# Optimization experiments

Measured on AMD Instinct MI355X. Metric: run time of the kernel, lower is better.

The kernel has to match this reference:

```python
import jax, jax.numpy as jnp
import numpy as np

N_QUBITS = 10
QLCU_LAYERS = 2
FEATURE_DIM = 256
BATCH = 256
N_PARAMS = 5 * N_QUBITS * QLCU_LAYERS  # 100
TWO_PI = 2.0 * np.pi


def _rx_mat(theta):
    # (B,) -> (B,2,2) complex64
    c = jnp.cos(theta / 2).astype(jnp.complex64)
    s = (-1j * jnp.sin(theta / 2)).astype(jnp.complex64)
    return jnp.stack([jnp.stack([c, s], -1), jnp.stack([s, c], -1)], -2)


def _ry_mat(theta):
    c = jnp.cos(theta / 2).astype(jnp.complex64)
    s = jnp.sin(theta / 2).astype(jnp.complex64)
    return jnp.stack([jnp.stack([c, -s], -1), jnp.stack([s, c], -1)], -2)


def _rz_mat(theta):
    e0 = jnp.exp(-0.5j * theta.astype(jnp.complex64))
    e1 = jnp.exp(0.5j * theta.astype(jnp.complex64))
    z = jnp.zeros_like(e0)
    return jnp.stack([jnp.stack([e0, z], -1), jnp.stack([z, e1], -1)], -2)


def _apply_1q(state, U, w):
    # state: (B,)+(2,)*n ; U: (B,2,2) ; wire w (PennyLane wire 0 = most significant)
    s = jnp.moveaxis(state, 1 + w, -1)
    s = jnp.einsum('bij,b...j->b...i', U, s)
    return jnp.moveaxis(s, -1, 1 + w)


def _apply_crx(state, theta, c, t):
    # controlled-RX: apply RX(theta) on target t where control c == 1
    s = jnp.moveaxis(state, (1 + c, 1 + t), (-2, -1))
    U = _rx_mat(theta)
    s1 = jnp.einsum('bij,b...j->b...i', U, s[..., 1, :])
    s = jnp.stack([s[..., 0, :], s1], axis=-2)
    return jnp.moveaxis(s, (-2, -1), (1 + c, 1 + t))


def _circuit(params):
    # params: (B, N_PARAMS) angles. Returns (B, 3*n) expvals [X.., Y.., Z..]
    n = N_QUBITS
    B = params.shape[0]
    state = jnp.zeros((B,) + (2,) * n, jnp.complex64)
    state = state.at[(slice(None),) + (0,) * n].set(1.0)
    idx = 0
    for _ in range(QLCU_LAYERS):
        for i in range(n):
            state = _apply_1q(state, _rx_mat(params[:, idx]), i)
            state = _apply_1q(state, _ry_mat(params[:, idx + 1]), i)
            state = _apply_1q(state, _rz_mat(params[:, idx + 2]), i)
            idx += 3
        for i in range(n):
            state = _apply_crx(state, params[:, idx], i, (i + 1) % n)
            idx += 1
        for i in range(n - 1, -1, -1):
            state = _apply_crx(state, params[:, idx], i, (i - 1) % n)
            idx += 1
    X, Y, Z = [], [], []
    for w in range(n):
        s = jnp.moveaxis(state, 1 + w, -1).reshape(B, -1, 2)
        z01 = jnp.sum(jnp.conj(s[..., 0]) * s[..., 1], axis=1)  # (B,)
        X.append(2.0 * jnp.real(z01))
        Y.append(2.0 * jnp.imag(z01))
        probs = jnp.sum(jnp.abs(s) ** 2, axis=1)  # (B,2)
        Z.append(probs[:, 0] - probs[:, 1])
    return jnp.stack(X + Y + Z, axis=1).astype(jnp.float32)


def _branch(x, W, b, base):
    p = x @ W.T + b            # (B, N_PARAMS)
    p = p + base[None, :]
    p = jax.nn.sigmoid(p) * TWO_PI
    return _circuit(p)


def setup_inputs() -> dict:
    key = jax.random.key(0)
    ks = jax.random.split(key, 16)
    d = {
        'x': jax.random.normal(ks[0], (BATCH, FEATURE_DIM), jnp.float32),
        'W1': jax.random.normal(ks[1], (N_PARAMS, FEATURE_DIM), jnp.float32) * 0.05,
        'b1': jnp.zeros((N_PARAMS,), jnp.float32),
        'W2': jax.random.normal(ks[2], (N_PARAMS, FEATURE_DIM), jnp.float32) * 0.05,
        'b2': jnp.zeros((N_PARAMS,), jnp.float32),
        'W3': jax.random.normal(ks[3], (N_PARAMS, FEATURE_DIM), jnp.float32) * 0.05,
        'b3': jnp.zeros((N_PARAMS,), jnp.float32),
        'base1': jax.random.uniform(ks[4], (N_PARAMS,), jnp.float32) * TWO_PI,
        'base2': jax.random.uniform(ks[5], (N_PARAMS,), jnp.float32) * TWO_PI,
        'base3': jax.random.uniform(ks[6], (N_PARAMS,), jnp.float32) * TWO_PI,
        'alpha_real': jax.random.uniform(ks[7], (1,), jnp.float32),
        'alpha_imag': jnp.zeros((1,), jnp.float32),
        'beta_real': jax.random.uniform(ks[8], (1,), jnp.float32),
        'beta_imag': jnp.zeros((1,), jnp.float32),
        'gamma_real': jax.random.uniform(ks[9], (1,), jnp.float32),
        'gamma_imag': jnp.zeros((1,), jnp.float32),
    }
    return d


def reference(x, W1, b1, W2, b2, W3, b3, base1, base2, base3,
              alpha_real, alpha_imag, beta_real, beta_imag, gamma_real, gamma_imag):
    m1 = _branch(x, W1, b1, base1)  # (B, 3n)
    m2 = _branch(x, W2, b2, base2)
    m3 = _branch(x, W3, b3, base3)
    norm = jnp.sqrt(alpha_real**2 + alpha_imag**2 + beta_real**2 + beta_imag**2
                    + gamma_real**2 + gamma_imag**2 + 1e-9)
    ar, ai = alpha_real / norm, alpha_imag / norm
    br, bi = beta_real / norm, beta_imag / norm
    gr, gi = gamma_real / norm, gamma_imag / norm
    re = ar * m1 + br * m2 + gr * m3
    im = ai * m1 + bi * m2 + gi * m3
    return jnp.sqrt(re * re + im * im)
```

## Files before the change

kernel.cpp:

```cpp
#include <hip/hip_runtime.h>
#include <math.h>

#define NQ 10
#define NPAR 100
#define FDIM 256
#define BATCH 256
#define NOUT 30
#define TWO_PI_F 6.283185307179586f


__device__ __forceinline__ float shx(float v, int mask) {
    return __shfl_xor(v, mask, 64);
}

__device__ __forceinline__ float2 cmul(float2 a, float2 b) {
    return make_float2(a.x*b.x - a.y*b.y, a.x*b.y + a.y*b.x);
}

template<int BIT>
__device__ __forceinline__ void gate1q(float2 (&st)[16], int lane,
                                       float2 u00, float2 u01, float2 u10, float2 u11)
{
    if constexpr (BIT >= 6) {
        constexpr int rb = 1 << (BIT - 6);
        #pragma unroll
        for (int a = 0; a < 16; ++a) {
            if (a & rb) continue;
            const int a1 = a | rb;
            const float2 A0 = st[a], A1 = st[a1];
            float2 n0, n1;
            n0.x = u00.x*A0.x - u00.y*A0.y + u01.x*A1.x - u01.y*A1.y;
            n0.y = u00.x*A0.y + u00.y*A0.x + u01.x*A1.y + u01.y*A1.x;
            n1.x = u10.x*A0.x - u10.y*A0.y + u11.x*A1.x - u11.y*A1.y;
            n1.y = u10.x*A0.y + u10.y*A0.x + u11.x*A1.y + u11.y*A1.x;
            st[a] = n0; st[a1] = n1;
        }
    } else {
        constexpr int lb = 1 << BIT;
        const bool hi = (lane & lb) != 0;
        const float2 A = hi ? u11 : u00;
        const float2 B = hi ? u10 : u01;
        #pragma unroll
        for (int a = 0; a < 16; ++a) {
            const float2 m = st[a];
            float2 p;
            p.x = shx(m.x, lb); p.y = shx(m.y, lb);
            float2 n;
            n.x = A.x*m.x - A.y*m.y + B.x*p.x - B.y*p.y;
            n.y = A.x*m.y + A.y*m.x + B.x*p.y + B.y*p.x;
            st[a] = n;
        }
    }
}

template<int BC, int BT>
__device__ __forceinline__ void crx(float2 (&st)[16], int lane, float c, float s)
{
    if constexpr (BT >= 6) {
        constexpr int rt = 1 << (BT - 6);
        if constexpr (BC >= 6) {
            constexpr int rc = 1 << (BC - 6);
            #pragma unroll
            for (int a = 0; a < 16; ++a) {
                if (!(a & rc) || (a & rt)) continue;
                const int a1 = a | rt;
                const float2 A0 = st[a], A1 = st[a1];
                float2 n0, n1;
                n0.x = c*A0.x + s*A1.y;  n0.y = c*A0.y - s*A1.x;
                n1.x = c*A1.x + s*A0.y;  n1.y = c*A1.y - s*A0.x;
                st[a] = n0; st[a1] = n1;
            }
        } else {
            constexpr int lc = 1 << BC;
            const bool act = (lane & lc) != 0;
            const float cc = act ? c : 1.f;
            const float ss = act ? s : 0.f;
            #pragma unroll
            for (int a = 0; a < 16; ++a) {
                if (a & rt) continue;
                const int a1 = a | rt;
                const float2 A0 = st[a], A1 = st[a1];
                float2 n0, n1;
                n0.x = cc*A0.x + ss*A1.y;  n0.y = cc*A0.y - ss*A1.x;
                n1.x = cc*A1.x + ss*A0.y;  n1.y = cc*A1.y - ss*A0.x;
                st[a] = n0; st[a1] = n1;
            }
        }
    } else {
        constexpr int lt = 1 << BT;
        float cc, ss;
        if constexpr (BC < 6) {
            constexpr int lc = 1 << BC;
            const bool act = (lane & lc) != 0;
            cc = act ? c : 1.f;
            ss = act ? s : 0.f;
        } else { cc = c; ss = s; }
        #pragma unroll
        for (int a = 0; a < 16; ++a) {
            if constexpr (BC >= 6) {
                constexpr int rc = 1 << (BC - 6);
                if (!(a & rc)) continue;
            }
            const float2 m = st[a];
            float2 p;
            p.x = shx(m.x, lt); p.y = shx(m.y, lt);
            float2 n;
            n.x = cc*m.x + ss*p.y;
            n.y = cc*m.y - ss*p.x;
            st[a] = n;
        }
    }
}

template<int Q>
__device__ __forceinline__ void layer1q(float2 (&st)[16], int lane, const float2* cs, int idx)
{
    if constexpr (Q < NQ) {
        const float2 X = cs[idx], Y = cs[idx + 1], Z = cs[idx + 2];
        const float cx = X.x, sx = X.y, cy = Y.x, sy = Y.y, cz = Z.x, sz = Z.y;
        const float2 m00 = make_float2( cy*cx,  sy*sx);
        const float2 m01 = make_float2(-sy*cx, -cy*sx);
        const float2 m10 = make_float2( sy*cx, -cy*sx);
        const float2 m11 = make_float2( cy*cx, -sy*sx);
        const float2 u00 = make_float2(cz*m00.x + sz*m00.y, cz*m00.y - sz*m00.x);
        const float2 u01 = make_float2(cz*m01.x + sz*m01.y, cz*m01.y - sz*m01.x);
        const float2 u10 = make_float2(cz*m10.x - sz*m10.y, cz*m10.y + sz*m10.x);
        const float2 u11 = make_float2(cz*m11.x - sz*m11.y, cz*m11.y + sz*m11.x);
        gate1q<9 - Q>(st, lane, u00, u01, u10, u11);
        layer1q<Q + 1>(st, lane, cs, idx + 3);
    }
}

template<int Q>
__device__ __forceinline__ void ringF(float2 (&st)[16], int lane, const float2* cs, int idx)
{
    if constexpr (Q < NQ) {
        const float2 p = cs[idx];
        crx<9 - Q, 9 - ((Q + 1) % NQ)>(st, lane, p.x, p.y);
        ringF<Q + 1>(st, lane, cs, idx + 1);
    }
}

template<int Q>
__device__ __forceinline__ void ringB(float2 (&st)[16], int lane, const float2* cs, int idx)
{
    if constexpr (Q >= 0) {
        const float2 p = cs[idx];
        crx<9 - Q, 9 - ((Q + NQ - 1) % NQ)>(st, lane, p.x, p.y);
        ringB<Q - 1>(st, lane, cs, idx + 1);
    }
}

__device__ __forceinline__ void col0(const float2* cs, int w, float2& u00, float2& u10)
{
    const float2 X = cs[3*w], Y = cs[3*w + 1], Z = cs[3*w + 2];
    const float cx = X.x, sx = X.y, cy = Y.x, sy = Y.y, cz = Z.x, sz = Z.y;
    const float2 m00 = make_float2(cy*cx,  sy*sx);
    const float2 m10 = make_float2(sy*cx, -cy*sx);
    u00 = make_float2(cz*m00.x + sz*m00.y, cz*m00.y - sz*m00.x);
    u10 = make_float2(cz*m10.x - sz*m10.y, cz*m10.y + sz*m10.x);
}

template<int W>
__device__ __forceinline__ void measureAll(const float2 (&st)[16], int lane, float* m_row)
{
    if constexpr (W < NQ) {
        constexpr int B = 9 - W;
        float sre = 0.f, smm = 0.f, szz = 0.f;
        if constexpr (B >= 6) {
            constexpr int rb = 1 << (B - 6);
            #pragma unroll
            for (int a = 0; a < 16; ++a) {
                if (a & rb) continue;
                const int a1 = a | rb;
                const float2 A0 = st[a], A1 = st[a1];
                sre += A0.x*A1.x + A0.y*A1.y;
                smm += A0.x*A1.y - A0.y*A1.x;
                szz += A0.x*A0.x + A0.y*A0.y - A1.x*A1.x - A1.y*A1.y;
            }
            sre *= 2.f; smm *= 2.f;
        } else {
            constexpr int lb = 1 << B;
            const float sgn = (lane & lb) ? -1.f : 1.f;
            #pragma unroll
            for (int a = 0; a < 16; ++a) {
                const float2 m = st[a];
                float2 p;
                p.x = shx(m.x, lb); p.y = shx(m.y, lb);
                sre += m.x*p.x + m.y*p.y;
                smm += sgn * (m.x*p.y - m.y*p.x);
                szz += sgn * (m.x*m.x + m.y*m.y - p.x*p.x - p.y*p.y);
            }
            szz *= 0.5f;
        }
        #pragma unroll
        for (int off = 1; off < 64; off <<= 1) {
            sre += shx(sre, off);
            smm += shx(smm, off);
            szz += shx(szz, off);
        }
        if (lane == 0) {
            m_row[W]      = sre;
            m_row[10 + W] = smm;
            m_row[20 + W] = szz;
        }
        measureAll<W + 1>(st, lane, m_row);
    }
}

__global__ __launch_bounds__(192) void qsb_fused(
    const float* __restrict__ x,
    const float* __restrict__ W1, const float* __restrict__ b1, const float* __restrict__ base1,
    const float* __restrict__ W2, const float* __restrict__ b2, const float* __restrict__ base2,
    const float* __restrict__ W3, const float* __restrict__ b3, const float* __restrict__ base3,
    const float* __restrict__ ar_, const float* __restrict__ ai_,
    const float* __restrict__ br_, const float* __restrict__ bi_,
    const float* __restrict__ gr_, const float* __restrict__ gi_,
    float* __restrict__ out)
{
    const int b    = blockIdx.x;
    const int wv   = threadIdx.x >> 6;
    const int lane = threadIdx.x & 63;

    const float* W    = (wv == 0) ? W1    : (wv == 1) ? W2    : W3;
    const float* bias = (wv == 0) ? b1    : (wv == 1) ? b2    : b3;
    const float* base = (wv == 0) ? base1 : (wv == 1) ? base2 : base3;

    __shared__ float2 css[3][NPAR];
    __shared__ float  mloc[3][NOUT];
    float2* cs = css[wv];

    if (lane < 50) {
        const int p0 = 2 * lane;
        const float4* xr = reinterpret_cast<const float4*>(x + (size_t)b * FDIM);
        const float4* w0 = reinterpret_cast<const float4*>(W + (size_t)p0 * FDIM);
        const float4* w1 = reinterpret_cast<const float4*>(W + (size_t)(p0 + 1) * FDIM);
        float acc0 = 0.f, acc1 = 0.f;
        #pragma unroll 8
        for (int k = 0; k < FDIM / 4; ++k) {
            const float4 xv = xr[k];
            const float4 a  = w0[k];
            const float4 bb = w1[k];
            acc0 += xv.x*a.x  + xv.y*a.y  + xv.z*a.z  + xv.w*a.w;
            acc1 += xv.x*bb.x + xv.y*bb.y + xv.z*bb.z + xv.w*bb.w;
        }
        acc0 += bias[p0]     + base[p0];
        acc1 += bias[p0 + 1] + base[p0 + 1];
        const float t0 = TWO_PI_F / (1.f + __expf(-acc0));
        const float t1 = TWO_PI_F / (1.f + __expf(-acc1));
        float s0, c0, s1, c1;
        __sincosf(0.5f * t0, &s0, &c0);
        __sincosf(0.5f * t1, &s1, &c1);
        cs[p0]     = make_float2(c0, s0);
        cs[p0 + 1] = make_float2(c1, s1);
    }
    __syncthreads();

    float2 st[16];
    {
        float2 lp = make_float2(1.f, 0.f);
        #pragma unroll
        for (int bb = 0; bb < 6; ++bb) {
            float2 u00, u10;
            col0(cs, 9 - bb, u00, u10);
            const float2 sel = ((lane >> bb) & 1) ? u10 : u00;
            lp = cmul(lp, sel);
        }
        float2 v3[2], v2[2], v1[2], v0[2];
        col0(cs, 3, v3[0], v3[1]);
        col0(cs, 2, v2[0], v2[1]);
        col0(cs, 1, v1[0], v1[1]);
        col0(cs, 0, v0[0], v0[1]);
        #pragma unroll
        for (int a = 0; a < 16; ++a) {
            float2 t = cmul(v3[a & 1], v2[(a >> 1) & 1]);
            t = cmul(t, cmul(v1[(a >> 2) & 1], v0[(a >> 3) & 1]));
            st[a] = cmul(t, lp);
        }
    }

    ringF<0>(st, lane, cs, 30);
    ringB<NQ - 1>(st, lane, cs, 40);
    layer1q<0>(st, lane, cs, 50);
    ringF<0>(st, lane, cs, 80);
    ringB<NQ - 1>(st, lane, cs, 90);

    measureAll<0>(st, lane, mloc[wv]);
    __syncthreads();

    if (threadIdx.x < NOUT) {
        const int i = threadIdx.x;
        const float ar = ar_[0], ai = ai_[0];
        const float br = br_[0], bi = bi_[0];
        const float gr = gr_[0], gi = gi_[0];
        const float inv = 1.f / sqrtf(ar*ar + ai*ai + br*br + bi*bi
                                      + gr*gr + gi*gi + 1e-9f);
        const float m1 = mloc[0][i], m2 = mloc[1][i], m3 = mloc[2][i];
        const float re = (ar * m1 + br * m2 + gr * m3) * inv;
        const float im = (ai * m1 + bi * m2 + gi * m3) * inv;
        out[(size_t)b * NOUT + i] = sqrtf(re * re + im * im);
    }
}

extern "C" void kernel_launch(void* const* d_in, const int* in_sizes, int n_in,
                              void* d_out, int out_size, void* d_ws, size_t ws_size,
                              hipStream_t stream)
{
    (void)in_sizes; (void)n_in; (void)out_size; (void)d_ws; (void)ws_size;
    const float* x     = (const float*)d_in[0];
    const float* W1    = (const float*)d_in[1];
    const float* b1    = (const float*)d_in[2];
    const float* W2    = (const float*)d_in[3];
    const float* b2    = (const float*)d_in[4];
    const float* W3    = (const float*)d_in[5];
    const float* b3    = (const float*)d_in[6];
    const float* base1 = (const float*)d_in[7];
    const float* base2 = (const float*)d_in[8];
    const float* base3 = (const float*)d_in[9];
    const float* ar    = (const float*)d_in[10];
    const float* ai    = (const float*)d_in[11];
    const float* br    = (const float*)d_in[12];
    const float* bi    = (const float*)d_in[13];
    const float* gr    = (const float*)d_in[14];
    const float* gi    = (const float*)d_in[15];

    qsb_fused<<<dim3(BATCH), dim3(192), 0, stream>>>(
        x, W1, b1, base1, W2, b2, base2, W3, b3, base3,
        ar, ai, br, bi, gr, gi, (float*)d_out);
}
```

Baseline: 117.3 us.

## Split each circuit state across two wavefronts and use DPP/swizzle lane exchanges

Each branch's 1024-amplitude state is now split across two wavefronts with 8 slots per lane instead of one wavefront with 16. Qubit 9 becomes the wave index, and gates on it exchange amplitudes through shared memory with block barriers. Shuffle-xor is replaced by DPP and ds_swizzle intrinsics for lane masks below 32. The linear projection is spread over 100 threads and the measurement reduction now produces four partial sums per branch. The goal is more parallelism and lower register pressure, at the cost of many __syncthreads on the qubit-9 gates.

```diff
diff --git a/kernel.cpp b/kernel.cpp
--- a/kernel.cpp
+++ b/kernel.cpp
@@ -7,24 +7,161 @@
 #define BATCH 256
 #define NOUT 30
 #define TWO_PI_F 6.283185307179586f
-
-
-__device__ __forceinline__ float shx(float v, int mask) {
-    return __shfl_xor(v, mask, 64);
+#define NSLOT 8
+
+
+template<int MASK>
+__device__ __forceinline__ float lx(float v) {
+    if constexpr (MASK == 1) {
+        return __int_as_float(__builtin_amdgcn_update_dpp(
+            0, __float_as_int(v), 0xB1, 0xF, 0xF, true));
+    } else if constexpr (MASK == 2) {
+        return __int_as_float(__builtin_amdgcn_update_dpp(
+            0, __float_as_int(v), 0x4E, 0xF, 0xF, true));
+    } else if constexpr (MASK == 8) {
+        return __int_as_float(__builtin_amdgcn_update_dpp(
+            0, __float_as_int(v), 0x128, 0xF, 0xF, true));
+    } else if constexpr (MASK == 4) {
+        return __int_as_float(__builtin_amdgcn_ds_swizzle(__float_as_int(v), 0x101F));
+    } else if constexpr (MASK == 16) {
+        return __int_as_float(__builtin_amdgcn_ds_swizzle(__float_as_int(v), 0x401F));
+    } else {
+        return __shfl_xor(v, 32, 64);
+    }
+}
+
+template<int MASK>
+__device__ __forceinline__ float2 lx2(float2 v) {
+    return make_float2(lx<MASK>(v.x), lx<MASK>(v.y));
 }
 
 __device__ __forceinline__ float2 cmul(float2 a, float2 b) {
     return make_float2(a.x*b.x - a.y*b.y, a.x*b.y + a.y*b.x);
 }
 
+struct Ctx {
+    int lane;
+    int W;
+    float2* exs;
+    float2* exp_;
+};
+
+template<int BC, int BT>
+__device__ __forceinline__ void crx(float2 (&st)[NSLOT], const Ctx& cx, float c, float s)
+{
+    if constexpr (BT == 9) {
+        if constexpr (BC >= 6) {
+            constexpr int rc = 1 << (BC - 6);
+            #pragma unroll
+            for (int a = 0; a < NSLOT; ++a) if (a & rc) cx.exs[a] = st[a];
+            __syncthreads();
+            #pragma unroll
+            for (int a = 0; a < NSLOT; ++a) if (a & rc) {
+                const float2 p = cx.exp_[a]; const float2 m = st[a];
+                st[a] = make_float2(c*m.x + s*p.y, c*m.y - s*p.x);
+            }
+            __syncthreads();
+        } else {
+            #pragma unroll
+            for (int a = 0; a < NSLOT; ++a) cx.exs[a] = st[a];
+            __syncthreads();
+            const bool act = (cx.lane >> BC) & 1;
+            const float cc = act ? c : 1.f, ss = act ? s : 0.f;
+            #pragma unroll
+            for (int a = 0; a < NSLOT; ++a) {
+                const float2 p = cx.exp_[a]; const float2 m = st[a];
+                st[a] = make_float2(cc*m.x + ss*p.y, cc*m.y - ss*p.x);
+            }
+            __syncthreads();
+        }
+    } else if constexpr (BC == 9) {
+        if (cx.W) {
+            if constexpr (BT >= 6) {
+                constexpr int rt = 1 << (BT - 6);
+                #pragma unroll
+                for (int a = 0; a < NSLOT; ++a) {
+                    if (a & rt) continue;
+                    const int a1 = a | rt;
+                    const float2 A0 = st[a], A1 = st[a1];
+                    st[a]  = make_float2(c*A0.x + s*A1.y, c*A0.y - s*A1.x);
+                    st[a1] = make_float2(c*A1.x + s*A0.y, c*A1.y - s*A0.x);
+                }
+            } else {
+                constexpr int M = 1 << BT;
+                #pragma unroll
+                for (int a = 0; a < NSLOT; ++a) {
+                    const float2 p = lx2<M>(st[a]); const float2 m = st[a];
+                    st[a] = make_float2(c*m.x + s*p.y, c*m.y - s*p.x);
+                }
+            }
+        }
+    } else if constexpr (BT >= 6) {
+        constexpr int rt = 1 << (BT - 6);
+        if constexpr (BC >= 6) {
+            constexpr int rc = 1 << (BC - 6);
+            #pragma unroll
+            for (int a = 0; a < NSLOT; ++a) {
+                if (!(a & rc) || (a & rt)) continue;
+                const int a1 = a | rt;
+                const float2 A0 = st[a], A1 = st[a1];
+                st[a]  = make_float2(c*A0.x + s*A1.y, c*A0.y - s*A1.x);
+                st[a1] = make_float2(c*A1.x + s*A0.y, c*A1.y - s*A0.x);
+            }
+        } else {
+            const bool act = (cx.lane >> BC) & 1;
+            const float cc = act ? c : 1.f, ss = act ? s : 0.f;
+            #pragma unroll
+            for (int a = 0; a < NSLOT; ++a) {
+                if (a & rt) continue;
+                const int a1 = a | rt;
+                const float2 A0 = st[a], A1 = st[a1];
+                st[a]  = make_float2(cc*A0.x + ss*A1.y, cc*A0.y - ss*A1.x);
+                st[a1] = make_float2(cc*A1.x + ss*A0.y, cc*A1.y - ss*A0.x);
+            }
+        }
+    } else {
+        constexpr int M = 1 << BT;
+        if constexpr (BC >= 6) {
+            constexpr int rc = 1 << (BC - 6);
+            #pragma unroll
+            for (int a = 0; a < NSLOT; ++a) {
+                if (!(a & rc)) continue;
+                const float2 p = lx2<M>(st[a]); const float2 m = st[a];
+                st[a] = make_float2(c*m.x + s*p.y, c*m.y - s*p.x);
+            }
+        } else {
+            const bool act = (cx.lane >> BC) & 1;
+            const float cc = act ? c : 1.f, ss = act ? s : 0.f;
+            #pragma unroll
+            for (int a = 0; a < NSLOT; ++a) {
+                const float2 p = lx2<M>(st[a]); const float2 m = st[a];
+                st[a] = make_float2(cc*m.x + ss*p.y, cc*m.y - ss*p.x);
+            }
+        }
+    }
+}
+
 template<int BIT>
-__device__ __forceinline__ void gate1q(float2 (&st)[16], int lane,
+__device__ __forceinline__ void gate1q(float2 (&st)[NSLOT], const Ctx& cx,
                                        float2 u00, float2 u01, float2 u10, float2 u11)
 {
-    if constexpr (BIT >= 6) {
+    if constexpr (BIT == 9) {
+        #pragma unroll
+        for (int a = 0; a < NSLOT; ++a) cx.exs[a] = st[a];
+        __syncthreads();
+        const float2 A = cx.W ? u11 : u00;
+        const float2 B = cx.W ? u10 : u01;
+        #pragma unroll
+        for (int a = 0; a < NSLOT; ++a) {
+            const float2 m = st[a]; const float2 p = cx.exp_[a];
+            st[a] = make_float2(A.x*m.x - A.y*m.y + B.x*p.x - B.y*p.y,
+                                A.x*m.y + A.y*m.x + B.x*p.y + B.y*p.x);
+        }
+        __syncthreads();
+    } else if constexpr (BIT >= 6) {
         constexpr int rb = 1 << (BIT - 6);
         #pragma unroll
-        for (int a = 0; a < 16; ++a) {
+        for (int a = 0; a < NSLOT; ++a) {
             if (a & rb) continue;
             const int a1 = a | rb;
             const float2 A0 = st[a], A1 = st[a1];
@@ -36,118 +173,58 @@
             st[a] = n0; st[a1] = n1;
         }
     } else {
-        constexpr int lb = 1 << BIT;
-        const bool hi = (lane & lb) != 0;
+        constexpr int M = 1 << BIT;
+        const bool hi = (cx.lane >> BIT) & 1;
         const float2 A = hi ? u11 : u00;
         const float2 B = hi ? u10 : u01;
         #pragma unroll
-        for (int a = 0; a < 16; ++a) {
-            const float2 m = st[a];
-            float2 p;
-            p.x = shx(m.x, lb); p.y = shx(m.y, lb);
-            float2 n;
-            n.x = A.x*m.x - A.y*m.y + B.x*p.x - B.y*p.y;
-            n.y = A.x*m.y + A.y*m.x + B.x*p.y + B.y*p.x;
-            st[a] = n;
-        }
-    }
-}
-
-template<int BC, int BT>
-__device__ __forceinline__ void crx(float2 (&st)[16], int lane, float c, float s)
-{
-    if constexpr (BT >= 6) {
-        constexpr int rt = 1 << (BT - 6);
-        if constexpr (BC >= 6) {
-            constexpr int rc = 1 << (BC - 6);
-            #pragma unroll
-            for (int a = 0; a < 16; ++a) {
-                if (!(a & rc) || (a & rt)) continue;
-                const int a1 = a | rt;
-                const float2 A0 = st[a], A1 = st[a1];
-                float2 n0, n1;
-                n0.x = c*A0.x + s*A1.y;  n0.y = c*A0.y - s*A1.x;
-                n1.x = c*A1.x + s*A0.y;  n1.y = c*A1.y - s*A0.x;
-                st[a] = n0; st[a1] = n1;
-            }
-        } else {
-            constexpr int lc = 1 << BC;
-            const bool act = (lane & lc) != 0;
-            const float cc = act ? c : 1.f;
-            const float ss = act ? s : 0.f;
-            #pragma unroll
-            for (int a = 0; a < 16; ++a) {
-                if (a & rt) continue;
-                const int a1 = a | rt;
-                const float2 A0 = st[a], A1 = st[a1];
-                float2 n0, n1;
-                n0.x = cc*A0.x + ss*A1.y;  n0.y = cc*A0.y - ss*A1.x;
-                n1.x = cc*A1.x + ss*A0.y;  n1.y = cc*A1.y - ss*A0.x;
-                st[a] = n0; st[a1] = n1;
-            }
-        }
-    } else {
-        constexpr int lt = 1 << BT;
-        float cc, ss;
-        if constexpr (BC < 6) {
-            constexpr int lc = 1 << BC;
-            const bool act = (lane & lc) != 0;
-            cc = act ? c : 1.f;
-            ss = act ? s : 0.f;
-        } else { cc = c; ss = s; }
-        #pragma unroll
-        for (int a = 0; a < 16; ++a) {
-            if constexpr (BC >= 6) {
-                constexpr int rc = 1 << (BC - 6);
-                if (!(a & rc)) continue;
-            }
-            const float2 m = st[a];
-            float2 p;
-            p.x = shx(m.x, lt); p.y = shx(m.y, lt);
-            float2 n;
-            n.x = cc*m.x + ss*p.y;
-            n.y = cc*m.y - ss*p.x;
-            st[a] = n;
+        for (int a = 0; a < NSLOT; ++a) {
+            const float2 p = lx2<M>(st[a]); const float2 m = st[a];
+            st[a] = make_float2(A.x*m.x - A.y*m.y + B.x*p.x - B.y*p.y,
+                                A.x*m.y + A.y*m.x + B.x*p.y + B.y*p.x);
         }
     }
 }
 
 template<int Q>
-__device__ __forceinline__ void layer1q(float2 (&st)[16], int lane, const float2* cs, int idx)
+__device__ __forceinline__ void layer1q(float2 (&st)[NSLOT], const Ctx& cx,
+                                        const float2* cs, int idx)
 {
     if constexpr (Q < NQ) {
         const float2 X = cs[idx], Y = cs[idx + 1], Z = cs[idx + 2];
-        const float cx = X.x, sx = X.y, cy = Y.x, sy = Y.y, cz = Z.x, sz = Z.y;
-        const float2 m00 = make_float2( cy*cx,  sy*sx);
-        const float2 m01 = make_float2(-sy*cx, -cy*sx);
-        const float2 m10 = make_float2( sy*cx, -cy*sx);
-        const float2 m11 = make_float2( cy*cx, -sy*sx);
+        const float cx_ = X.x, sx = X.y, cy = Y.x, sy = Y.y, cz = Z.x, sz = Z.y;
+        const float2 m00 = make_float2( cy*cx_,  sy*sx);
+        const float2 m01 = make_float2(-sy*cx_, -cy*sx);
+        const float2 m10 = make_float2( sy*cx_, -cy*sx);
+        const float2 m11 = make_float2( cy*cx_, -sy*sx);
         const float2 u00 = make_float2(cz*m00.x + sz*m00.y, cz*m00.y - sz*m00.x);
         const float2 u01 = make_float2(cz*m01.x + sz*m01.y, cz*m01.y - sz*m01.x);
         const float2 u10 = make_float2(cz*m10.x - sz*m10.y, cz*m10.y + sz*m10.x);
         const float2 u11 = make_float2(cz*m11.x - sz*m11.y, cz*m11.y + sz*m11.x);
-        gate1q<9 - Q>(st, lane, u00, u01, u10, u11);
-        layer1q<Q + 1>(st, lane, cs, idx + 3);
+        gate1q<9 - Q>(st, cx, u00, u01, u10, u11);
+        layer1q<Q + 1>(st, cx, cs, idx + 3);
     }
 }
 
 template<int Q>
-__device__ __forceinline__ void ringF(float2 (&st)[16], int lane, const float2* cs, int idx)
+__device__ __forceinline__ void ringF(float2 (&st)[NSLOT], const Ctx& cx,
+                                      const float2* cs, int idx)
 {
     if constexpr (Q < NQ) {
         const float2 p = cs[idx];
-        crx<9 - Q, 9 - ((Q + 1) % NQ)>(st, lane, p.x, p.y);
-        ringF<Q + 1>(st, lane, cs, idx + 1);
+        crx<9 - Q, 9 - ((Q + 1) % NQ)>(st, cx, p.x, p.y);
+        ringF<Q + 1>(st, cx, cs, idx + 1);
     }
 }
 
 template<int Q>
-__device__ __forceinline__ void ringB(float2 (&st)[16], int lane, const float2* cs, int idx)
+__device__ __forceinline__ void ringB(float2 (&st)[NSLOT], const Ctx& cx,
+                                      const float2* cs, int idx)
 {
     if constexpr (Q >= 0) {
         const float2 p = cs[idx];
-        crx<9 - Q, 9 - ((Q + NQ - 1) % NQ)>(st, lane, p.x, p.y);
-        ringB<Q - 1>(st, lane, cs, idx + 1);
+        crx<9 - Q, 9 - ((Q + NQ - 1) % NQ)>(st, cx, p.x, p.y);
+        ringB<Q - 1>(st, cx, cs, idx + 1);
     }
 }
 
@@ -161,16 +238,30 @@
     u10 = make_float2(cz*m10.x - sz*m10.y, cz*m10.y + sz*m10.x);
 }
 
-template<int W>
-__device__ __forceinline__ void measureAll(const float2 (&st)[16], int lane, float* m_row)
-{
-    if constexpr (W < NQ) {
-        constexpr int B = 9 - W;
+template<int Wq>
+__device__ __forceinline__ void measureAll(const float2 (&st)[NSLOT], const Ctx& cx,
+                                           float* mrow )
+{
+    if constexpr (Wq < NQ) {
+        constexpr int B = 9 - Wq;
         float sre = 0.f, smm = 0.f, szz = 0.f;
-        if constexpr (B >= 6) {
+        if constexpr (B == 9) {
+            #pragma unroll
+            for (int a = 0; a < NSLOT; ++a) cx.exs[a] = st[a];
+            __syncthreads();
+            const float sgn = cx.W ? -1.f : 1.f;
+            #pragma unroll
+            for (int a = 0; a < NSLOT; ++a) {
+                const float2 m = st[a], p = cx.exp_[a];
+                sre += m.x*p.x + m.y*p.y;
+                smm += sgn * (m.x*p.y - m.y*p.x);
+                szz += sgn * (m.x*m.x + m.y*m.y);
+            }
+            __syncthreads();
+        } else if constexpr (B >= 6) {
             constexpr int rb = 1 << (B - 6);
             #pragma unroll
-            for (int a = 0; a < 16; ++a) {
+            for (int a = 0; a < NSLOT; ++a) {
                 if (a & rb) continue;
                 const int a1 = a | rb;
                 const float2 A0 = st[a], A1 = st[a1];
@@ -180,35 +271,32 @@
             }
             sre *= 2.f; smm *= 2.f;
         } else {
-            constexpr int lb = 1 << B;
-            const float sgn = (lane & lb) ? -1.f : 1.f;
-            #pragma unroll
-            for (int a = 0; a < 16; ++a) {
+            constexpr int M = 1 << B;
+            const float sgn = ((cx.lane >> B) & 1) ? -1.f : 1.f;
+            #pragma unroll
+            for (int a = 0; a < NSLOT; ++a) {
                 const float2 m = st[a];
-                float2 p;
-                p.x = shx(m.x, lb); p.y = shx(m.y, lb);
+                const float2 p = lx2<M>(m);
                 sre += m.x*p.x + m.y*p.y;
                 smm += sgn * (m.x*p.y - m.y*p.x);
                 szz += sgn * (m.x*m.x + m.y*m.y - p.x*p.x - p.y*p.y);
             }
             szz *= 0.5f;
         }
-        #pragma unroll
-        for (int off = 1; off < 64; off <<= 1) {
-            sre += shx(sre, off);
-            smm += shx(smm, off);
-            szz += shx(szz, off);
-        }
-        if (lane == 0) {
-            m_row[W]      = sre;
-            m_row[10 + W] = smm;
-            m_row[20 + W] = szz;
-        }
-        measureAll<W + 1>(st, lane, m_row);
-    }
-}
-
-__global__ __launch_bounds__(192) void qsb_fused(
+        sre += lx<1>(sre); sre += lx<2>(sre); sre += lx<4>(sre); sre += lx<8>(sre); sre += lx<16>(sre);
+        smm += lx<1>(smm); smm += lx<2>(smm); smm += lx<4>(smm); smm += lx<8>(smm); smm += lx<16>(smm);
+        szz += lx<1>(szz); szz += lx<2>(szz); szz += lx<4>(szz); szz += lx<8>(szz); szz += lx<16>(szz);
+        if ((cx.lane & 31) == 0) {
+            const int k = (cx.W << 1) | (cx.lane >> 5);
+            mrow[k * NOUT + Wq]      = sre;
+            mrow[k * NOUT + 10 + Wq] = smm;
+            mrow[k * NOUT + 20 + Wq] = szz;
+        }
+        measureAll<Wq + 1>(st, cx, mrow);
+    }
+}
+
+__global__ __launch_bounds__(384) void qsb_fused(
     const float* __restrict__ x,
     const float* __restrict__ W1, const float* __restrict__ b1, const float* __restrict__ base1,
     const float* __restrict__ W2, const float* __restrict__ b2, const float* __restrict__ base2,
@@ -219,86 +307,91 @@
     float* __restrict__ out)
 {
     const int b    = blockIdx.x;
-    const int wv   = threadIdx.x >> 6;
+    const int wv2  = threadIdx.x >> 6;
+    const int br   = wv2 >> 1;
+    const int W    = wv2 & 1;
     const int lane = threadIdx.x & 63;
-
-    const float* W    = (wv == 0) ? W1    : (wv == 1) ? W2    : W3;
-    const float* bias = (wv == 0) ? b1    : (wv == 1) ? b2    : b3;
-    const float* base = (wv == 0) ? base1 : (wv == 1) ? base2 : base3;
+    const int lt   = (W << 6) | lane;
+
+    const float* Wp   = (br == 0) ? W1    : (br == 1) ? W2    : W3;
+    const float* bias = (br == 0) ? b1    : (br == 1) ? b2    : b3;
+    const float* base = (br == 0) ? base1 : (br == 1) ? base2 : base3;
 
     __shared__ float2 css[3][NPAR];
-    __shared__ float  mloc[3][NOUT];
-    float2* cs = css[wv];
-
-    if (lane < 50) {
-        const int p0 = 2 * lane;
+    __shared__ float2 exb[3][2][64][9];
+    __shared__ float  mred[3][4][NOUT];
+
+    if (lt < NPAR) {
         const float4* xr = reinterpret_cast<const float4*>(x + (size_t)b * FDIM);
-        const float4* w0 = reinterpret_cast<const float4*>(W + (size_t)p0 * FDIM);
-        const float4* w1 = reinterpret_cast<const float4*>(W + (size_t)(p0 + 1) * FDIM);
-        float acc0 = 0.f, acc1 = 0.f;
+        const float4* wr = reinterpret_cast<const float4*>(Wp + (size_t)lt * FDIM);
+        float acc = 0.f;
         #pragma unroll 8
         for (int k = 0; k < FDIM / 4; ++k) {
             const float4 xv = xr[k];
-            const float4 a  = w0[k];
-            const float4 bb = w1[k];
-            acc0 += xv.x*a.x  + xv.y*a.y  + xv.z*a.z  + xv.w*a.w;
-            acc1 += xv.x*bb.x + xv.y*bb.y + xv.z*bb.z + xv.w*bb.w;
-        }
-        acc0 += bias[p0]     + base[p0];
-        acc1 += bias[p0 + 1] + base[p0 + 1];
-        const float t0 = TWO_PI_F / (1.f + __expf(-acc0));
-        const float t1 = TWO_PI_F / (1.f + __expf(-acc1));
-        float s0, c0, s1, c1;
-        __sincosf(0.5f * t0, &s0, &c0);
-        __sincosf(0.5f * t1, &s1, &c1);
-        cs[p0]     = make_float2(c0, s0);
-        cs[p0 + 1] = make_float2(c1, s1);
+            const float4 wv4 = wr[k];
+            acc += xv.x*wv4.x + xv.y*wv4.y + xv.z*wv4.z + xv.w*wv4.w;
+        }
+        acc += bias[lt] + base[lt];
+        const float t = TWO_PI_F / (1.f + __expf(-acc));
+        float sn, cn;
+        __sincosf(0.5f * t, &sn, &cn);
+        css[br][lt] = make_float2(cn, sn);
     }
     __syncthreads();
 
-    float2 st[16];
+    const float2* cs = css[br];
+    Ctx cx;
+    cx.lane = lane; cx.W = W;
+    cx.exs  = &exb[br][W][lane][0];
+    cx.exp_ = &exb[br][1 - W][lane][0];
+
+    float2 st[NSLOT];
     {
         float2 lp = make_float2(1.f, 0.f);
         #pragma unroll
         for (int bb = 0; bb < 6; ++bb) {
             float2 u00, u10;
             col0(cs, 9 - bb, u00, u10);
-            const float2 sel = ((lane >> bb) & 1) ? u10 : u00;
-            lp = cmul(lp, sel);
-        }
-        float2 v3[2], v2[2], v1[2], v0[2];
-        col0(cs, 3, v3[0], v3[1]);
-        col0(cs, 2, v2[0], v2[1]);
-        col0(cs, 1, v1[0], v1[1]);
-        col0(cs, 0, v0[0], v0[1]);
-        #pragma unroll
-        for (int a = 0; a < 16; ++a) {
-            float2 t = cmul(v3[a & 1], v2[(a >> 1) & 1]);
-            t = cmul(t, cmul(v1[(a >> 2) & 1], v0[(a >> 3) & 1]));
+            lp = cmul(lp, ((lane >> bb) & 1) ? u10 : u00);
+        }
+        {
+            float2 u00, u10;
+            col0(cs, 0, u00, u10);
+            lp = cmul(lp, W ? u10 : u00);
+        }
+        float2 v0[2], v1[2], v2[2];
+        col0(cs, 3, v0[0], v0[1]);
+        col0(cs, 2, v1[0], v1[1]);
+        col0(cs, 1, v2[0], v2[1]);
+        #pragma unroll
+        for (int a = 0; a < NSLOT; ++a) {
+            const float2 t = cmul(v0[a & 1], cmul(v1[(a >> 1) & 1], v2[(a >> 2) & 1]));
             st[a] = cmul(t, lp);
         }
     }
 
-    ringF<0>(st, lane, cs, 30);
-    ringB<NQ - 1>(st, lane, cs, 40);
-    layer1q<0>(st, lane, cs, 50);
-    ringF<0>(st, lane, cs, 80);
-    ringB<NQ - 1>(st, lane, cs, 90);
-
-    measureAll<0>(st, lane, mloc[wv]);
+    ringF<0>(st, cx, cs, 30);
+    ringB<NQ - 1>(st, cx, cs, 40);
+    layer1q<0>(st, cx, cs, 50);
+    ringF<0>(st, cx, cs, 80);
+    ringB<NQ - 1>(st, cx, cs, 90);
+
+    measureAll<0>(st, cx, &mred[br][0][0]);
     __syncthreads();
 
     if (threadIdx.x < NOUT) {
-        const int i = threadIdx.x;
+        const int j = threadIdx.x;
+        const float m1 = mred[0][0][j] + mred[0][1][j] + mred[0][2][j] + mred[0][3][j];
+        const float m2 = mred[1][0][j] + mred[1][1][j] + mred[1][2][j] + mred[1][3][j];
+        const float m3 = mred[2][0][j] + mred[2][1][j] + mred[2][2][j] + mred[2][3][j];
         const float ar = ar_[0], ai = ai_[0];
-        const float br = br_[0], bi = bi_[0];
+        const float brr = br_[0], bii = bi_[0];
         const float gr = gr_[0], gi = gi_[0];
-        const float inv = 1.f / sqrtf(ar*ar + ai*ai + br*br + bi*bi
+        const float inv = 1.f / sqrtf(ar*ar + ai*ai + brr*brr + bii*bii
                                       + gr*gr + gi*gi + 1e-9f);
-        const float m1 = mloc[0][i], m2 = mloc[1][i], m3 = mloc[2][i];
-        const float re = (ar * m1 + br * m2 + gr * m3) * inv;
-        const float im = (ai * m1 + bi * m2 + gi * m3) * inv;
-        out[(size_t)b * NOUT + i] = sqrtf(re * re + im * im);
+        const float re = (ar * m1 + brr * m2 + gr * m3) * inv;
+        const float im = (ai * m1 + bii * m2 + gi * m3) * inv;
+        out[(size_t)b * NOUT + j] = sqrtf(re * re + im * im);
     }
 }
 
@@ -324,7 +417,7 @@
     const float* gr    = (const float*)d_in[14];
     const float* gi    = (const float*)d_in[15];
 
-    qsb_fused<<<dim3(BATCH), dim3(192), 0, stream>>>(
+    qsb_fused<<<dim3(BATCH), dim3(384), 0, stream>>>(
         x, W1, b1, base1, W2, b2, base2, W3, b3, base3,
         ar, ai, br, bi, gr, gi, (float*)d_out);
 }
```

New measurement: 108.5 us, median of 2. -7.5%, faster.
